# Kernel tuning notes

Hardware: AMD Instinct MI355X
Metric: run time of the kernel (lower is better)

## Reference

```python
import jax, jax.numpy as jnp
import numpy as np

B, N = 4096, 64
EPS = 1e-6
LANE = np.array([13.55, 17.45, 21.12, 24.91], dtype=np.float32)


def _lin_params(key, out_f, in_f):
    k1, k2 = jax.random.split(key)
    bound = 1.0 / np.sqrt(in_f)
    W = jax.random.uniform(k1, (out_f, in_f), jnp.float32, -bound, bound)
    b = jax.random.uniform(k2, (out_f,), jnp.float32, -bound, bound)
    return W, b


def setup_inputs() -> dict:
    key = jax.random.key(0)
    ks = jax.random.split(key, 16)
    inp = {
        "ego_y": jax.random.uniform(ks[0], (B,), jnp.float32, 10.0, 28.0),
        "Pn": jax.random.normal(ks[1], (B, N, 2), jnp.float32),
        "Pego": jax.random.normal(ks[2], (B, 2), jnp.float32),
        "Vn": jax.random.normal(ks[3], (B, N, 2), jnp.float32),
        "Vego": jax.random.normal(ks[4], (B, 2), jnp.float32),
        "Cn": jax.random.normal(ks[5], (B, N, 2), jnp.float32),
    }
    inp["W_sel"], inp["b_sel"] = _lin_params(ks[6], 4, 4)
    inp["W_s0"], inp["b_s0"] = _lin_params(ks[7], 8, 4)      # aug_sin0
    inp["W_map"], inp["b_map"] = _lin_params(ks[8], 8, 48)   # Er map
    inp["W_efc"], inp["b_efc"] = _lin_params(ks[9], 2, 8)
    inp["W_s1"], inp["b_s1"] = _lin_params(ks[10], 17, 2)    # aug_sin1
    inp["W1"], inp["b1"] = _lin_params(ks[11], 256, 114)     # En_mlp
    inp["W2"], inp["b2"] = _lin_params(ks[12], 128, 256)
    inp["W3"], inp["b3"] = _lin_params(ks[13], 2, 128)
    inp["Ww"], inp["bw"] = _lin_params(ks[14], 1, 6)
    return inp


def _leaky(x):
    return jnp.where(x >= 0, x, 0.1 * x)


def _auge(data, W_sin, b_sin):
    # data: [..., d]; returns concat of 10 feature blocks along last axis
    sin = jnp.sin(data @ W_sin.T + b_sin) + EPS
    sqr = data ** 2 + EPS
    cub = data ** 3 + EPS
    exp = jnp.exp(data) + EPS
    inv = 1.0 / (data + EPS)
    return jnp.concatenate(
        [data, sin, sqr, cub, exp, inv, 1.0 / sin, 1.0 / sqr, 1.0 / cub, 1.0 / exp],
        axis=-1,
    )


def reference(ego_y, Pn, Pego, Vn, Vego, Cn,
              W_sel, b_sel, W_s0, b_s0, W_map, b_map, W_efc, b_efc,
              W_s1, b_s1, W1, b1, W2, b2, W3, b3, Ww, bw):
    lane = jnp.asarray(LANE)
    # ---- Er_net (batched over B) ----
    delta_y = lane[None, :] - ego_y[:, None]                      # [B,4]
    x = jax.nn.softmax(delta_y @ W_sel.T + b_sel, axis=-1) * delta_y
    x = _auge(x, W_s0, b_s0)                                      # [B,48]
    x = _leaky(x @ W_map.T + b_map)                               # [B,8]
    Er = x @ W_efc.T + b_efc                                      # [B,2]

    # ---- En_net (batched over B, vectorized over N neighbors) ----
    Pego_r = jnp.broadcast_to(Pego[:, None, :], (B, N, 2))
    Vego_r = jnp.broadcast_to(Vego[:, None, :], (B, N, 2))
    dP = Pn - Pego_r
    dV = Vn - Vego_r
    dP_aug = _auge(dP, W_s1, b_s1)                                # [B,N,50]
    dV_aug = _auge(dV, W_s1, b_s1)                                # [B,N,50]
    Ninfo = jnp.concatenate(
        [Pego_r, Pn, dP, dP_aug, Vego_r, Vn, dV, dV_aug, Cn], axis=-1
    )                                                             # [B,N,114]
    h = _leaky(Ninfo @ W1.T + b1)                                 # [B,N,256]
    h = _leaky(h @ W2.T + b2)                                     # [B,N,128]
    En = h @ W3.T + b3                                            # [B,N,2]
    logits = jnp.concatenate([En, Pn, dP], axis=-1) @ Ww.T + bw   # [B,N,1]
    weight = jax.nn.softmax(logits, axis=1)                       # softmax over neighbors
    En_out = jnp.sum(weight * En, axis=1)                         # [B,2]

    return jnp.concatenate([Er, En_out], axis=-1)                 # [B,4]
```

## Files before the change

kernel.cpp:

```cpp
#include <hip/hip_runtime.h>
#include <math.h>

#define EPS 1e-6f
#define NB 4096
#define NN 64

typedef __attribute__((ext_vector_type(8))) short short8_t;
typedef __attribute__((ext_vector_type(4))) float f32x4;
typedef __attribute__((ext_vector_type(4))) unsigned u32x4;
typedef __attribute__((ext_vector_type(2))) unsigned u32x2;

__device__ __forceinline__ unsigned cvtpk(float a, float b) {
  unsigned r;
  asm("v_cvt_pk_bf16_f32 %0, %1, %2" : "=v"(r) : "v"(a), "v"(b));
  return r;
}
__device__ __forceinline__ unsigned split2(float a, float b, unsigned& lo) {
  unsigned h = cvtpk(a, b);
  float ra = __uint_as_float(h << 16);
  float rb = __uint_as_float(h & 0xFFFF0000u);
  lo = cvtpk(a - ra, b - rb);
  return h;
}

__global__ __launch_bounds__(64)
void w_prep_kernel(const float* __restrict__ W1,
                   const float* __restrict__ W2,
                   short* __restrict__ W1F,
                   short* __restrict__ W2F) {
  const int g = blockIdx.x;
  const int l = threadIdx.x;
  float v[8];
  if (g < 64) {
    int mt = g >> 2, ks = g & 3;
    int m = mt * 16 + (l & 15), k0 = ks * 32 + (l >> 4) * 8;
#pragma unroll
    for (int j = 0; j < 8; j++)
      v[j] = (k0 + j < 114) ? W1[m * 114 + k0 + j] : 0.0f;
    u32x4 hi, lo;
#pragma unroll
    for (int i = 0; i < 4; i++) {
      unsigned lt;
      hi[i] = split2(v[2 * i], v[2 * i + 1], lt);
      lo[i] = lt;
    }
    int base = ((mt * 4 + ks) * 64 + l) * 16;
    *(u32x4*)&W1F[base] = hi;
    *(u32x4*)&W1F[base + 8] = lo;
  } else {
    int t = g - 64;
    int mt = t >> 3, ks = t & 7;
    int m = mt * 16 + (l & 15), k0 = ks * 32 + (l >> 4) * 8;
#pragma unroll
    for (int j = 0; j < 8; j++) v[j] = W2[m * 256 + k0 + j];
    u32x4 hi, lo;
#pragma unroll
    for (int i = 0; i < 4; i++) {
      unsigned lt;
      hi[i] = split2(v[2 * i], v[2 * i + 1], lt);
      lo[i] = lt;
    }
    int base = ((mt * 8 + ks) * 64 + l) * 16;
    *(u32x4*)&W2F[base] = hi;
    *(u32x4*)&W2F[base + 8] = lo;
  }
}

__global__ __launch_bounds__(512, 4)
void en_kernel(const float* __restrict__ Pn, const float* __restrict__ Pego,
               const float* __restrict__ Vn, const float* __restrict__ Vego,
               const float* __restrict__ Cn,
               const float* __restrict__ W_s1, const float* __restrict__ b_s1,
               const float* __restrict__ b1, const float* __restrict__ b2,
               const float* __restrict__ W3, const float* __restrict__ b3,
               const float* __restrict__ Ww, const float* __restrict__ bw,
               const float* __restrict__ ego_y,
               const float* __restrict__ W_sel, const float* __restrict__ b_sel,
               const float* __restrict__ W_s0, const float* __restrict__ b_s0,
               const float* __restrict__ W_map, const float* __restrict__ b_map,
               const float* __restrict__ W_efc, const float* __restrict__ b_efc,
               const short* __restrict__ W1F, const short* __restrict__ W2F,
               float* __restrict__ out) {
  __shared__ __align__(16) short uni[64 * 512];
  __shared__ float stash[4 * 64];
  __shared__ float w3s[256];
  __shared__ float b1s[256];
  __shared__ float b2s[128];
  __shared__ float en_part[4][64][2];

  const int b = blockIdx.x;
  const int tid = threadIdx.x;
  const int w = tid >> 6;
  const int l = tid & 63;
  const int lr = l & 15;
  const int lq = l >> 4;
  const int ntb = (w >> 2) * 2;

  if (tid < 256) { w3s[tid] = W3[tid]; b1s[tid] = b1[tid]; }
  else if (tid < 384) b2s[tid - 256] = b2[tid - 256];

  {
    const int r = l;
    const int rsw = (r & 7) << 3;
    auto putg = [&](int g, const float* v) {
      u32x4 hi, lo;
#pragma unroll
      for (int i = 0; i < 4; i++) {
        unsigned lt;
        hi[i] = split2(v[2 * i], v[2 * i + 1], lt);
        lo[i] = lt;
      }
      int idx = r * 256 + ((g * 8) ^ rsw);
      *(u32x4*)&uni[idx] = hi;
      *(u32x4*)&uni[idx + 128] = lo;
    };
    if (w == 6) {
      const float2 p2 = ((const float2*)Pn)[b * NN + r];
      float e0 = Pego[b * 2 + 0], e1 = Pego[b * 2 + 1];
      stash[0 * 64 + r] = p2.x; stash[1 * 64 + r] = p2.y;
      stash[2 * 64 + r] = p2.x - e0; stash[3 * 64 + r] = p2.y - e1;
      const float2 cn = ((const float2*)Cn)[b * NN + r];
      float g14[8] = {cn.x, cn.y, 0.f, 0.f, 0.f, 0.f, 0.f, 0.f};
      float g15[8] = {0.f, 0.f, 0.f, 0.f, 0.f, 0.f, 0.f, 0.f};
      putg(14, g14);
      putg(15, g15);
    } else if (w < 6) {
      const bool isV = (w >= 3);
      const int role = isV ? (w - 3) : w;
      const int gb = isV ? 7 : 0;
      const float2 p2 = ((const float2*)(isV ? Vn : Pn))[b * NN + r];
      const float* Eb = isV ? Vego : Pego;
      float e0 = Eb[b * 2 + 0], e1 = Eb[b * 2 + 1];
      float d0 = p2.x - e0, d1 = p2.y - e1;
      if (role == 0) {
        float a15 = fmaf(W_s1[30], d0, fmaf(W_s1[31], d1, b_s1[15]));
        float a16 = fmaf(W_s1[32], d0, fmaf(W_s1[33], d1, b_s1[16]));
        float s15 = sinf(a15) + EPS, s16 = sinf(a16) + EPS;
        float q0 = d0 * d0 + EPS, q1 = d1 * d1 + EPS;
        float c30 = (d0 * d0) * d0 + EPS, c31 = (d1 * d1) * d1 + EPS;
        float ex0 = expf(d0) + EPS, ex1 = expf(d1) + EPS;
        float g0[8] = {e0, e1, p2.x, p2.y, d0, d1, d0, d1};
        float g3[8] = {s16, q0, q1, c30, c31, ex0, ex1, 1.0f / (d0 + EPS)};
        float g6[8] = {1.0f / s15, 1.0f / s16, 1.0f / q0, 1.0f / q1,
                       1.0f / c30, 1.0f / c31, 1.0f / ex0, 1.0f / ex1};
        putg(gb + 0, g0);
        putg(gb + 3, g3);
        putg(gb + 6, g6);
      } else if (role == 1) {
        float s[8];
#pragma unroll
        for (int i = 0; i < 8; i++) {
          float a = fmaf(W_s1[2 * i], d0, fmaf(W_s1[2 * i + 1], d1, b_s1[i]));
          s[i] = sinf(a) + EPS;
        }
        float g1[8] = {s[0], s[1], s[2], s[3], s[4], s[5], s[6], s[7]};
        float g4[8] = {1.0f / (d1 + EPS), 1.0f / s[0], 1.0f / s[1], 1.0f / s[2],
                       1.0f / s[3], 1.0f / s[4], 1.0f / s[5], 1.0f / s[6]};
        putg(gb + 1, g1);
        putg(gb + 4, g4);
      } else {
        float s[9];
#pragma unroll
        for (int i = 0; i < 9; i++) {
          float a = fmaf(W_s1[2 * (7 + i)], d0,
                         fmaf(W_s1[2 * (7 + i) + 1], d1, b_s1[7 + i]));
          s[i] = sinf(a) + EPS;
        }
        float g2[8] = {s[1], s[2], s[3], s[4], s[5], s[6], s[7], s[8]};
        float g5[8] = {1.0f / s[0], 1.0f / s[1], 1.0f / s[2], 1.0f / s[3],
                       1.0f / s[4], 1.0f / s[5], 1.0f / s[6], 1.0f / s[7]};
        putg(gb + 2, g2);
        putg(gb + 5, g5);
      }
    } else if (l < 8) {
      const int sub = l;
      const float lane4[4] = {13.55f, 17.45f, 21.12f, 24.91f};
      float ego = ego_y[b];
      float dy[4];
#pragma unroll
      for (int j = 0; j < 4; j++) dy[j] = lane4[j] - ego;
      float t[4];
#pragma unroll
      for (int i = 0; i < 4; i++) {
        float a = b_sel[i];
#pragma unroll
        for (int j = 0; j < 4; j++) a = fmaf(W_sel[i * 4 + j], dy[j], a);
        t[i] = a;
      }
      float m = fmaxf(fmaxf(t[0], t[1]), fmaxf(t[2], t[3]));
      float e[4], s = 0.f;
#pragma unroll
      for (int i = 0; i < 4; i++) { e[i] = expf(t[i] - m); s += e[i]; }
      float x[4];
#pragma unroll
      for (int i = 0; i < 4; i++) x[i] = (e[i] / s) * dy[i];
      float f[48];
      float sn[8];
#pragma unroll
      for (int k = 0; k < 8; k++) {
        float a = b_s0[k];
#pragma unroll
        for (int j = 0; j < 4; j++) a = fmaf(W_s0[k * 4 + j], x[j], a);
        sn[k] = sinf(a) + EPS;
      }
#pragma unroll
      for (int i = 0; i < 4; i++) f[i] = x[i];
#pragma unroll
      for (int k = 0; k < 8; k++) f[4 + k] = sn[k];
#pragma unroll
      for (int i = 0; i < 4; i++) {
        float q = x[i] * x[i] + EPS;
        f[12 + i] = q; f[36 + i] = 1.0f / q;
      }
#pragma unroll
      for (int i = 0; i < 4; i++) {
        float c3 = (x[i] * x[i]) * x[i] + EPS;
        f[16 + i] = c3; f[40 + i] = 1.0f / c3;
      }
#pragma unroll
      for (int i = 0; i < 4; i++) {
        float ex = expf(x[i]) + EPS;
        f[20 + i] = ex; f[44 + i] = 1.0f / ex;
      }
#pragma unroll
      for (int i = 0; i < 4; i++) f[24 + i] = 1.0f / (x[i] + EPS);
#pragma unroll
      for (int k = 0; k < 8; k++) f[28 + k] = 1.0f / sn[k];
      float a = b_map[sub];
#pragma unroll
      for (int k = 0; k < 48; k++) a = fmaf(W_map[sub * 48 + k], f[k], a);
      float y = fmaxf(a, 0.1f * a);
      float t0 = W_efc[sub] * y;
      float t1 = W_efc[8 + sub] * y;
#pragma unroll
      for (int off = 4; off > 0; off >>= 1) {
        t0 += __shfl_xor(t0, off);
        t1 += __shfl_xor(t1, off);
      }
      if (sub == 0) {
        out[b * 4 + 0] = t0 + b_efc[0];
        out[b * 4 + 1] = t1 + b_efc[1];
      }
    }
  }
  __syncthreads();

  const short* w1b = W1F + l * 16;
  f32x4 acc1[4][2];
#pragma unroll
  for (int m = 0; m < 4; m++)
#pragma unroll
    for (int n = 0; n < 2; n++) acc1[m][n] = (f32x4)0.0f;

#pragma unroll
  for (int ks = 0; ks < 4; ks++) {
    short8_t w1h[4], w1l[4];
#pragma unroll
    for (int m = 0; m < 4; m++) {
      int fo = (((w & 3) * 4 + m) * 4 + ks) * 1024;
      w1h[m] = *(const short8_t*)&w1b[fo];
      w1l[m] = *(const short8_t*)&w1b[fo + 8];
    }
    short8_t bh[2], bl[2];
#pragma unroll
    for (int n = 0; n < 2; n++) {
      int rr = (ntb + n) * 16 + lr;
      int idx = rr * 256 + ((ks * 32 + lq * 8) ^ ((rr & 7) << 3));
      bh[n] = *(const short8_t*)&uni[idx];
      bl[n] = *(const short8_t*)&uni[idx + 128];
    }
    __builtin_amdgcn_s_setprio(1);
#pragma unroll
    for (int m = 0; m < 4; m++)
#pragma unroll
      for (int n = 0; n < 2; n++)
        acc1[m][n] = __builtin_amdgcn_mfma_f32_16x16x32_bf16(
            w1h[m], bh[n], acc1[m][n], 0, 0, 0);
#pragma unroll
    for (int m = 0; m < 4; m++)
#pragma unroll
      for (int n = 0; n < 2; n++)
        acc1[m][n] = __builtin_amdgcn_mfma_f32_16x16x32_bf16(
            w1h[m], bl[n], acc1[m][n], 0, 0, 0);
#pragma unroll
    for (int m = 0; m < 4; m++)
#pragma unroll
      for (int n = 0; n < 2; n++)
        acc1[m][n] = __builtin_amdgcn_mfma_f32_16x16x32_bf16(
            w1l[m], bh[n], acc1[m][n], 0, 0, 0);
    __builtin_amdgcn_s_setprio(0);
  }

  __syncthreads();

#pragma unroll
  for (int m = 0; m < 4; m++) {
    int o0 = ((w & 3) * 4 + m) * 16 + lq * 4;
    f32x4 bb = *(const f32x4*)&b1s[o0];
#pragma unroll
    for (int n = 0; n < 2; n++) {
      int rr = (ntb + n) * 16 + lr;
      float v0 = fmaxf(acc1[m][n][0] + bb[0], 0.1f * (acc1[m][n][0] + bb[0]));
      float v1 = fmaxf(acc1[m][n][1] + bb[1], 0.1f * (acc1[m][n][1] + bb[1]));
      float v2 = fmaxf(acc1[m][n][2] + bb[2], 0.1f * (acc1[m][n][2] + bb[2]));
      float v3 = fmaxf(acc1[m][n][3] + bb[3], 0.1f * (acc1[m][n][3] + bb[3]));
      u32x2 hi, lo;
      unsigned l0, l1;
      hi[0] = split2(v0, v1, l0);
      hi[1] = split2(v2, v3, l1);
      lo[0] = l0;
      lo[1] = l1;
      int idx = rr * 512 + (o0 ^ ((rr & 7) << 3));
      *(u32x2*)&uni[idx] = hi;
      *(u32x2*)&uni[idx + 256] = lo;
    }
  }
  __syncthreads();

  const short* w2b = W2F + l * 16;
  f32x4 acc2[2][2];
#pragma unroll
  for (int m = 0; m < 2; m++)
#pragma unroll
    for (int n = 0; n < 2; n++) acc2[m][n] = (f32x4)0.0f;

#pragma unroll
  for (int ks = 0; ks < 8; ks++) {
    short8_t w2h[2], w2l[2];
#pragma unroll
    for (int m = 0; m < 2; m++) {
      int fo = (((w & 3) * 2 + m) * 8 + ks) * 1024;
      w2h[m] = *(const short8_t*)&w2b[fo];
      w2l[m] = *(const short8_t*)&w2b[fo + 8];
    }
    short8_t bh[2], bl[2];
#pragma unroll
    for (int n = 0; n < 2; n++) {
      int rr = (ntb + n) * 16 + lr;
      int idx = rr * 512 + ((ks * 32 + lq * 8) ^ ((rr & 7) << 3));
      bh[n] = *(const short8_t*)&uni[idx];
      bl[n] = *(const short8_t*)&uni[idx + 256];
    }
    __builtin_amdgcn_s_setprio(1);
#pragma unroll
    for (int m = 0; m < 2; m++)
#pragma unroll
      for (int n = 0; n < 2; n++)
        acc2[m][n] = __builtin_amdgcn_mfma_f32_16x16x32_bf16(
            w2h[m], bh[n], acc2[m][n], 0, 0, 0);
#pragma unroll
    for (int m = 0; m < 2; m++)
#pragma unroll
      for (int n = 0; n < 2; n++)
        acc2[m][n] = __builtin_amdgcn_mfma_f32_16x16x32_bf16(
            w2h[m], bl[n], acc2[m][n], 0, 0, 0);
#pragma unroll
    for (int m = 0; m < 2; m++)
#pragma unroll
      for (int n = 0; n < 2; n++)
        acc2[m][n] = __builtin_amdgcn_mfma_f32_16x16x32_bf16(
            w2l[m], bh[n], acc2[m][n], 0, 0, 0);
    __builtin_amdgcn_s_setprio(0);
  }

  {
    f32x4 w3v[2][2];
#pragma unroll
    for (int c = 0; c < 2; c++)
#pragma unroll
      for (int m = 0; m < 2; m++)
        w3v[c][m] = *(const f32x4*)
            &w3s[c * 128 + ((w & 3) * 2 + m) * 16 + lq * 4];

    float p00 = 0.f, p01 = 0.f, p10 = 0.f, p11 = 0.f;
#pragma unroll
    for (int m = 0; m < 2; m++) {
      int o0 = ((w & 3) * 2 + m) * 16 + lq * 4;
      f32x4 bb = *(const f32x4*)&b2s[o0];
#pragma unroll
      for (int i = 0; i < 4; i++) {
        float u0 = acc2[m][0][i] + bb[i];
        u0 = fmaxf(u0, 0.1f * u0);
        float u1 = acc2[m][1][i] + bb[i];
        u1 = fmaxf(u1, 0.1f * u1);
        p00 = fmaf(u0, w3v[0][m][i], p00);
        p10 = fmaf(u0, w3v[1][m][i], p10);
        p01 = fmaf(u1, w3v[0][m][i], p01);
        p11 = fmaf(u1, w3v[1][m][i], p11);
      }
    }
#pragma unroll
    for (int off = 16; off < 64; off <<= 1) {
      p00 += __shfl_xor(p00, off);
      p01 += __shfl_xor(p01, off);
      p10 += __shfl_xor(p10, off);
      p11 += __shfl_xor(p11, off);
    }
    if (l < 16) {
      en_part[w & 3][ntb * 16 + l][0] = p00;
      en_part[w & 3][ntb * 16 + l][1] = p10;
      en_part[w & 3][(ntb + 1) * 16 + l][0] = p01;
      en_part[w & 3][(ntb + 1) * 16 + l][1] = p11;
    }
  }
  __syncthreads();

  if (tid < 64) {
    const int r = tid;
    float E0 = b3[0] + en_part[0][r][0] + en_part[1][r][0] +
               en_part[2][r][0] + en_part[3][r][0];
    float E1 = b3[1] + en_part[0][r][1] + en_part[1][r][1] +
               en_part[2][r][1] + en_part[3][r][1];
    float pn0 = stash[0 * 64 + r], pn1 = stash[1 * 64 + r];
    float dp0 = stash[2 * 64 + r], dp1 = stash[3 * 64 + r];
    float logit = bw[0];
    logit = fmaf(E0, Ww[0], logit);
    logit = fmaf(E1, Ww[1], logit);
    logit = fmaf(pn0, Ww[2], logit);
    logit = fmaf(pn1, Ww[3], logit);
    logit = fmaf(dp0, Ww[4], logit);
    logit = fmaf(dp1, Ww[5], logit);
    float m = logit;
#pragma unroll
    for (int off = 32; off > 0; off >>= 1) m = fmaxf(m, __shfl_xor(m, off));
    float e = expf(logit - m);
    float ssum = e;
#pragma unroll
    for (int off = 32; off > 0; off >>= 1) ssum += __shfl_xor(ssum, off);
    float wgt = e / ssum;
    float o0 = wgt * E0, o1 = wgt * E1;
#pragma unroll
    for (int off = 32; off > 0; off >>= 1) {
      o0 += __shfl_xor(o0, off);
      o1 += __shfl_xor(o1, off);
    }
    if (r == 0) {
      out[b * 4 + 2] = o0;
      out[b * 4 + 3] = o1;
    }
  }
}

extern "C" void kernel_launch(void* const* d_in, const int* in_sizes, int n_in,
                              void* d_out, int out_size, void* d_ws, size_t ws_size,
                              hipStream_t stream) {
  const float* ego_y = (const float*)d_in[0];
  const float* Pn    = (const float*)d_in[1];
  const float* Pego  = (const float*)d_in[2];
  const float* Vn    = (const float*)d_in[3];
  const float* Vego  = (const float*)d_in[4];
  const float* Cn    = (const float*)d_in[5];
  const float* W_sel = (const float*)d_in[6];
  const float* b_sel = (const float*)d_in[7];
  const float* W_s0  = (const float*)d_in[8];
  const float* b_s0  = (const float*)d_in[9];
  const float* W_map = (const float*)d_in[10];
  const float* b_map = (const float*)d_in[11];
  const float* W_efc = (const float*)d_in[12];
  const float* b_efc = (const float*)d_in[13];
  const float* W_s1  = (const float*)d_in[14];
  const float* b_s1  = (const float*)d_in[15];
  const float* W1    = (const float*)d_in[16];
  const float* b1    = (const float*)d_in[17];
  const float* W2    = (const float*)d_in[18];
  const float* b2    = (const float*)d_in[19];
  const float* W3    = (const float*)d_in[20];
  const float* b3    = (const float*)d_in[21];
  const float* Ww    = (const float*)d_in[22];
  const float* bw    = (const float*)d_in[23];
  float* out = (float*)d_out;

  short* W1F = (short*)d_ws;
  short* W2F = W1F + 65536;

  w_prep_kernel<<<128, 64, 0, stream>>>(W1, W2, W1F, W2F);
  en_kernel<<<NB, 512, 0, stream>>>(Pn, Pego, Vn, Vego, Cn, W_s1, b_s1,
                                    b1, b2, W3, b3, Ww, bw,
                                    ego_y, W_sel, b_sel, W_s0, b_s0,
                                    W_map, b_map, W_efc, b_efc,
                                    W1F, W2F, out);
}
```

Baseline: 218.4 us.

## Use hardware rcp/exp intrinsics and prefetch next-k weight fragments in MFMA loops

Replaces IEEE divisions and expf calls in the feature-augmentation and softmax code with raw v_rcp_f32 and v_exp_f32 instructions. This cuts the multi-instruction division and exp sequences at some cost in accuracy and denormal/edge handling. Separately, the W1 and W2 MFMA loops now load the next k-step's high weight fragments one iteration early, so global load latency overlaps with the current MFMAs. The prefetch adds register pressure.

Result: slower. 243.9 us (+11.7%).

```diff
diff --git a/kernel.cpp b/kernel.cpp
--- a/kernel.cpp
+++ b/kernel.cpp
@@ -21,6 +21,17 @@
   float rb = __uint_as_float(h & 0xFFFF0000u);
   lo = cvtpk(a - ra, b - rb);
   return h;
+}
+__device__ __forceinline__ float frcp(float x) {
+  float r;
+  asm("v_rcp_f32 %0, %1" : "=v"(r) : "v"(x));
+  return r;
+}
+__device__ __forceinline__ float fexp(float x) {
+  float t = x * 1.44269504088896f;
+  float r;
+  asm("v_exp_f32 %0, %1" : "=v"(r) : "v"(t));
+  return r;
 }
 
 __global__ __launch_bounds__(64)
@@ -138,11 +149,11 @@
         float s15 = sinf(a15) + EPS, s16 = sinf(a16) + EPS;
         float q0 = d0 * d0 + EPS, q1 = d1 * d1 + EPS;
         float c30 = (d0 * d0) * d0 + EPS, c31 = (d1 * d1) * d1 + EPS;
-        float ex0 = expf(d0) + EPS, ex1 = expf(d1) + EPS;
+        float ex0 = fexp(d0) + EPS, ex1 = fexp(d1) + EPS;
         float g0[8] = {e0, e1, p2.x, p2.y, d0, d1, d0, d1};
-        float g3[8] = {s16, q0, q1, c30, c31, ex0, ex1, 1.0f / (d0 + EPS)};
-        float g6[8] = {1.0f / s15, 1.0f / s16, 1.0f / q0, 1.0f / q1,
-                       1.0f / c30, 1.0f / c31, 1.0f / ex0, 1.0f / ex1};
+        float g3[8] = {s16, q0, q1, c30, c31, ex0, ex1, frcp(d0 + EPS)};
+        float g6[8] = {frcp(s15), frcp(s16), frcp(q0), frcp(q1),
+                       frcp(c30), frcp(c31), frcp(ex0), frcp(ex1)};
         putg(gb + 0, g0);
         putg(gb + 3, g3);
         putg(gb + 6, g6);
@@ -154,8 +165,8 @@
           s[i] = sinf(a) + EPS;
         }
         float g1[8] = {s[0], s[1], s[2], s[3], s[4], s[5], s[6], s[7]};
-        float g4[8] = {1.0f / (d1 + EPS), 1.0f / s[0], 1.0f / s[1], 1.0f / s[2],
-                       1.0f / s[3], 1.0f / s[4], 1.0f / s[5], 1.0f / s[6]};
+        float g4[8] = {frcp(d1 + EPS), frcp(s[0]), frcp(s[1]), frcp(s[2]),
+                       frcp(s[3]), frcp(s[4]), frcp(s[5]), frcp(s[6])};
         putg(gb + 1, g1);
         putg(gb + 4, g4);
       } else {
@@ -167,8 +178,8 @@
           s[i] = sinf(a) + EPS;
         }
         float g2[8] = {s[1], s[2], s[3], s[4], s[5], s[6], s[7], s[8]};
-        float g5[8] = {1.0f / s[0], 1.0f / s[1], 1.0f / s[2], 1.0f / s[3],
-                       1.0f / s[4], 1.0f / s[5], 1.0f / s[6], 1.0f / s[7]};
+        float g5[8] = {frcp(s[0]), frcp(s[1]), frcp(s[2]), frcp(s[3]),
+                       frcp(s[4]), frcp(s[5]), frcp(s[6]), frcp(s[7])};
         putg(gb + 2, g2);
         putg(gb + 5, g5);
       }
@@ -190,10 +201,11 @@
       float m = fmaxf(fmaxf(t[0], t[1]), fmaxf(t[2], t[3]));
       float e[4], s = 0.f;
 #pragma unroll
-      for (int i = 0; i < 4; i++) { e[i] = expf(t[i] - m); s += e[i]; }
+      for (int i = 0; i < 4; i++) { e[i] = fexp(t[i] - m); s += e[i]; }
+      float rs = frcp(s);
       float x[4];
 #pragma unroll
-      for (int i = 0; i < 4; i++) x[i] = (e[i] / s) * dy[i];
+      for (int i = 0; i < 4; i++) x[i] = (e[i] * rs) * dy[i];
       float f[48];
       float sn[8];
 #pragma unroll
@@ -210,22 +222,22 @@
 #pragma unroll
       for (int i = 0; i < 4; i++) {
         float q = x[i] * x[i] + EPS;
-        f[12 + i] = q; f[36 + i] = 1.0f / q;
+        f[12 + i] = q; f[36 + i] = frcp(q);
       }
 #pragma unroll
       for (int i = 0; i < 4; i++) {
         float c3 = (x[i] * x[i]) * x[i] + EPS;
-        f[16 + i] = c3; f[40 + i] = 1.0f / c3;
+        f[16 + i] = c3; f[40 + i] = frcp(c3);
       }
 #pragma unroll
       for (int i = 0; i < 4; i++) {
-        float ex = expf(x[i]) + EPS;
-        f[20 + i] = ex; f[44 + i] = 1.0f / ex;
-      }
-#pragma unroll
-      for (int i = 0; i < 4; i++) f[24 + i] = 1.0f / (x[i] + EPS);
-#pragma unroll
-      for (int k = 0; k < 8; k++) f[28 + k] = 1.0f / sn[k];
+        float ex = fexp(x[i]) + EPS;
+        f[20 + i] = ex; f[44 + i] = frcp(ex);
+      }
+#pragma unroll
+      for (int i = 0; i < 4; i++) f[24 + i] = frcp(x[i] + EPS);
+#pragma unroll
+      for (int k = 0; k < 8; k++) f[28 + k] = frcp(sn[k]);
       float a = b_map[sub];
 #pragma unroll
       for (int k = 0; k < 48; k++) a = fmaf(W_map[sub * 48 + k], f[k], a);
@@ -252,15 +264,23 @@
 #pragma unroll
     for (int n = 0; n < 2; n++) acc1[m][n] = (f32x4)0.0f;
 
+  short8_t ch[4];
+#pragma unroll
+  for (int m = 0; m < 4; m++)
+    ch[m] = *(const short8_t*)&w1b[(((w & 3) * 4 + m) * 4 + 0) * 1024];
+
 #pragma unroll
   for (int ks = 0; ks < 4; ks++) {
-    short8_t w1h[4], w1l[4];
-#pragma unroll
-    for (int m = 0; m < 4; m++) {
-      int fo = (((w & 3) * 4 + m) * 4 + ks) * 1024;
-      w1h[m] = *(const short8_t*)&w1b[fo];
-      w1l[m] = *(const short8_t*)&w1b[fo + 8];
-    }
+    short8_t nh[4];
+    if (ks < 3) {
+#pragma unroll
+      for (int m = 0; m < 4; m++)
+        nh[m] = *(const short8_t*)&w1b[(((w & 3) * 4 + m) * 4 + ks + 1) * 1024];
+    }
+    short8_t cl[4];
+#pragma unroll
+    for (int m = 0; m < 4; m++)
+      cl[m] = *(const short8_t*)&w1b[(((w & 3) * 4 + m) * 4 + ks) * 1024 + 8];
     short8_t bh[2], bl[2];
 #pragma unroll
     for (int n = 0; n < 2; n++) {
@@ -275,20 +295,24 @@
 #pragma unroll
       for (int n = 0; n < 2; n++)
         acc1[m][n] = __builtin_amdgcn_mfma_f32_16x16x32_bf16(
-            w1h[m], bh[n], acc1[m][n], 0, 0, 0);
+            ch[m], bh[n], acc1[m][n], 0, 0, 0);
 #pragma unroll
     for (int m = 0; m < 4; m++)
 #pragma unroll
       for (int n = 0; n < 2; n++)
         acc1[m][n] = __builtin_amdgcn_mfma_f32_16x16x32_bf16(
-            w1h[m], bl[n], acc1[m][n], 0, 0, 0);
+            ch[m], bl[n], acc1[m][n], 0, 0, 0);
 #pragma unroll
     for (int m = 0; m < 4; m++)
 #pragma unroll
       for (int n = 0; n < 2; n++)
         acc1[m][n] = __builtin_amdgcn_mfma_f32_16x16x32_bf16(
-            w1l[m], bh[n], acc1[m][n], 0, 0, 0);
+            cl[m], bh[n], acc1[m][n], 0, 0, 0);
     __builtin_amdgcn_s_setprio(0);
+    if (ks < 3) {
+#pragma unroll
+      for (int m = 0; m < 4; m++) ch[m] = nh[m];
+    }
   }
 
   __syncthreads();
@@ -324,15 +348,23 @@
 #pragma unroll
     for (int n = 0; n < 2; n++) acc2[m][n] = (f32x4)0.0f;
 
+  short8_t ch2[2];
+#pragma unroll
+  for (int m = 0; m < 2; m++)
+    ch2[m] = *(const short8_t*)&w2b[(((w & 3) * 2 + m) * 8 + 0) * 1024];
+
 #pragma unroll
   for (int ks = 0; ks < 8; ks++) {
-    short8_t w2h[2], w2l[2];
-#pragma unroll
-    for (int m = 0; m < 2; m++) {
-      int fo = (((w & 3) * 2 + m) * 8 + ks) * 1024;
-      w2h[m] = *(const short8_t*)&w2b[fo];
-      w2l[m] = *(const short8_t*)&w2b[fo + 8];
-    }
+    short8_t nh[2];
+    if (ks < 7) {
+#pragma unroll
+      for (int m = 0; m < 2; m++)
+        nh[m] = *(const short8_t*)&w2b[(((w & 3) * 2 + m) * 8 + ks + 1) * 1024];
+    }
+    short8_t cl[2];
+#pragma unroll
+    for (int m = 0; m < 2; m++)
+      cl[m] = *(const short8_t*)&w2b[(((w & 3) * 2 + m) * 8 + ks) * 1024 + 8];
     short8_t bh[2], bl[2];
 #pragma unroll
     for (int n = 0; n < 2; n++) {
@@ -347,20 +379,24 @@
 #pragma unroll
       for (int n = 0; n < 2; n++)
         acc2[m][n] = __builtin_amdgcn_mfma_f32_16x16x32_bf16(
-            w2h[m], bh[n], acc2[m][n], 0, 0, 0);
+            ch2[m], bh[n], acc2[m][n], 0, 0, 0);
 #pragma unroll
     for (int m = 0; m < 2; m++)
 #pragma unroll
       for (int n = 0; n < 2; n++)
         acc2[m][n] = __builtin_amdgcn_mfma_f32_16x16x32_bf16(
-            w2h[m], bl[n], acc2[m][n], 0, 0, 0);
+            ch2[m], bl[n], acc2[m][n], 0, 0, 0);
 #pragma unroll
     for (int m = 0; m < 2; m++)
 #pragma unroll
       for (int n = 0; n < 2; n++)
         acc2[m][n] = __builtin_amdgcn_mfma_f32_16x16x32_bf16(
-            w2l[m], bh[n], acc2[m][n], 0, 0, 0);
+            cl[m], bh[n], acc2[m][n], 0, 0, 0);
     __builtin_amdgcn_s_setprio(0);
+    if (ks < 7) {
+#pragma unroll
+      for (int m = 0; m < 2; m++) ch2[m] = nh[m];
+    }
   }
 
   {
@@ -423,11 +459,11 @@
     float m = logit;
 #pragma unroll
     for (int off = 32; off > 0; off >>= 1) m = fmaxf(m, __shfl_xor(m, off));
-    float e = expf(logit - m);
+    float e = fexp(logit - m);
     float ssum = e;
 #pragma unroll
     for (int off = 32; off > 0; off >>= 1) ssum += __shfl_xor(ssum, off);
-    float wgt = e / ssum;
+    float wgt = e * frcp(ssum);
     float o0 = wgt * E0, o1 = wgt * E1;
 #pragma unroll
     for (int off = 32; off > 0; off >>= 1) {
```
